# Kernel optimization log

Measured on AMD Instinct MI355X. Metric: run time of the kernel, lower is better.

Reference implementation:

```python
import jax, jax.numpy as jnp
import numpy as np

VOCAB = 50000
D = 300
S = 5
CTX = 10
B = 16384

def setup_inputs() -> dict:
    key = jax.random.key(0)
    k1, k2, k3 = jax.random.split(key, 3)
    x = jax.random.randint(k1, (B, 2 + CTX), 0, VOCAB, dtype=jnp.int32)
    W_g = jax.random.normal(k2, (VOCAB, D), dtype=jnp.float32)
    W_s = jax.random.normal(k3, (VOCAB, S, D), dtype=jnp.float32)
    return {"x": x, "W_g": W_g, "W_s": W_s}

def reference(x, W_g, W_s):
    # sum of context word global vectors: gather (B, CTX, D) -> sum -> (B, D)
    sum_context = jnp.sum(W_g[x[:, 2:]], axis=1)
    # sense vectors of target word: (B, S, D)
    sense_vecs = W_s[x[:, 0]]
    # per-sense dot with context (theano scan over senses): (S, B)
    scores = jnp.einsum('bsd,bd->sb', sense_vecs, sum_context)
    # (right_senses / context_sense_vectors are dead code in the original)
    # literal translation: sigmoid of sum over axis=1 of (S, B) -> (S,)
    return jax.nn.sigmoid(jnp.sum(scores, axis=1))
```

## Files before the change

kernel.cpp:

```cpp
#include <hip/hip_runtime.h>

typedef float v4f __attribute__((ext_vector_type(4)));

#define BATCH 16384
#define NS    5
#define NCTX  10
#define XSTR  (NCTX + 2)
#define D4    75
#define NBLK  4096

__global__ __launch_bounds__(256, 8) void sense_partials(
    const int*   __restrict__ x,
    const float* __restrict__ Wg,
    const float* __restrict__ Ws,
    float*       __restrict__ partial ) {
  const int lane = threadIdx.x & 63;
  const int wid  = threadIdx.x >> 6;
  const int b    = blockIdx.x * 4 + wid;

  const v4f* Wg4 = (const v4f*)Wg;
  const v4f* Ws4 = (const v4f*)Ws;

  int v = (lane < XSTR) ? x[(size_t)b * XSTR + lane] : 0;
  const int w0 = __shfl(v, 0);
  const v4f* wrow = Ws4 + (size_t)w0 * (NS * D4);

  const bool hi = (lane < D4 - 64);

  v4f sc0 = 0.f, sc1 = 0.f;
#pragma unroll
  for (int j = 0; j < NCTX; ++j) {
    const int c = __shfl(v, 2 + j);
    const v4f* r = Wg4 + (size_t)c * D4;
    sc0 += r[lane];
    if (hi) sc1 += r[64 + lane];
  }

  float acc[NS];
#pragma unroll
  for (int s = 0; s < NS; ++s) {
    v4f a0 = __builtin_nontemporal_load(&wrow[s * D4 + lane]);
    v4f p  = a0 * sc0;
    if (hi) {
      v4f a1 = __builtin_nontemporal_load(&wrow[s * D4 + 64 + lane]);
      p += a1 * sc1;
    }
    acc[s] = p.x + p.y + p.z + p.w;
  }

#pragma unroll
  for (int s = 0; s < NS; ++s) {
    float t = acc[s];
#pragma unroll
    for (int off = 32; off; off >>= 1) t += __shfl_down(t, off);
    acc[s] = t;
  }

  __shared__ float red[4][NS];
  if (lane == 0) {
#pragma unroll
    for (int s = 0; s < NS; ++s) red[wid][s] = acc[s];
  }
  __syncthreads();
  if (threadIdx.x < NS) {
    float t = red[0][threadIdx.x] + red[1][threadIdx.x] +
              red[2][threadIdx.x] + red[3][threadIdx.x];
    partial[threadIdx.x * NBLK + blockIdx.x] = t;
  }
}

__global__ __launch_bounds__(320) void sense_reduce(
    const float* __restrict__ partial, float* __restrict__ out) {
  const int lane = threadIdx.x & 63;
  const int s    = threadIdx.x >> 6;
  float sum = 0.f;
  for (int g = lane; g < NBLK; g += 64) sum += partial[s * NBLK + g];
#pragma unroll
  for (int off = 32; off; off >>= 1) sum += __shfl_down(sum, off);
  if (lane == 0) out[s] = 1.0f / (1.0f + __expf(-sum));
}

extern "C" void kernel_launch(void* const* d_in, const int* in_sizes, int n_in,
                              void* d_out, int out_size, void* d_ws, size_t ws_size,
                              hipStream_t stream) {
  const int*   x  = (const int*)d_in[0];
  const float* Wg = (const float*)d_in[1];
  const float* Ws = (const float*)d_in[2];
  float* partial  = (float*)d_ws;
  float* out      = (float*)d_out;

  sense_partials<<<NBLK, 256, 0, stream>>>(x, Wg, Ws, partial);
  sense_reduce<<<1, 320, 0, stream>>>(partial, out);
}
```

Baseline: 412.6 us.

## Process four batch rows per wavefront and pack tail columns across lanes

Each wavefront now handles four batch rows instead of one. The 11 leftover float4 columns of each row, beyond the first 64, are packed into lanes 0-43 so that lane utilization on the tail loads rises from 11/64 to 44/64. This raises memory-level parallelism per wave and cuts the block count to 1024 with lower occupancy bounds. In exchange it uses more registers and leaves fewer waves resident to hide latency.

```diff
diff --git a/kernel.cpp b/kernel.cpp
--- a/kernel.cpp
+++ b/kernel.cpp
@@ -7,44 +7,65 @@
 #define NCTX  10
 #define XSTR  (NCTX + 2)
 #define D4    75
-#define NBLK  4096
+#define HI    11
+#define NBLK  1024
 
-__global__ __launch_bounds__(256, 8) void sense_partials(
+__global__ __launch_bounds__(256, 4) void sense_partials(
     const int*   __restrict__ x,
     const float* __restrict__ Wg,
     const float* __restrict__ Ws,
     float*       __restrict__ partial ) {
   const int lane = threadIdx.x & 63;
   const int wid  = threadIdx.x >> 6;
-  const int b    = blockIdx.x * 4 + wid;
+  const int grp  = blockIdx.x * 4 + wid;
+  const int b0   = grp * 4;
 
   const v4f* Wg4 = (const v4f*)Wg;
   const v4f* Ws4 = (const v4f*)Ws;
 
-  int v = (lane < XSTR) ? x[(size_t)b * XSTR + lane] : 0;
-  const int w0 = __shfl(v, 0);
-  const v4f* wrow = Ws4 + (size_t)w0 * (NS * D4);
+  int v = (lane < 4 * XSTR) ? x[(size_t)b0 * XSTR + lane] : 0;
 
-  const bool hi = (lane < D4 - 64);
+  const int hr = lane / HI;
+  const int hc = lane - hr * HI;
+  const bool hiOn = (lane < 4 * HI);
 
-  v4f sc0 = 0.f, sc1 = 0.f;
+  int w0[4];
+#pragma unroll
+  for (int r = 0; r < 4; ++r) w0[r] = __shfl(v, r * XSTR);
+  const int wH = __shfl(v, hr * XSTR);
+
+  v4f s0[4] = {0.f, 0.f, 0.f, 0.f};
+  v4f sH    = 0.f;
+
 #pragma unroll
   for (int j = 0; j < NCTX; ++j) {
-    const int c = __shfl(v, 2 + j);
-    const v4f* r = Wg4 + (size_t)c * D4;
-    sc0 += r[lane];
-    if (hi) sc1 += r[64 + lane];
+    int c0 = __shfl(v, 0 * XSTR + 2 + j);
+    int c1 = __shfl(v, 1 * XSTR + 2 + j);
+    int c2 = __shfl(v, 2 * XSTR + 2 + j);
+    int c3 = __shfl(v, 3 * XSTR + 2 + j);
+    int cH = __shfl(v, hr * XSTR + 2 + j);
+    s0[0] += Wg4[(size_t)c0 * D4 + lane];
+    s0[1] += Wg4[(size_t)c1 * D4 + lane];
+    s0[2] += Wg4[(size_t)c2 * D4 + lane];
+    s0[3] += Wg4[(size_t)c3 * D4 + lane];
+    if (hiOn) sH += Wg4[(size_t)cH * D4 + 64 + hc];
   }
+
+  const v4f* wb0 = Ws4 + (size_t)w0[0] * (NS * D4);
+  const v4f* wb1 = Ws4 + (size_t)w0[1] * (NS * D4);
+  const v4f* wb2 = Ws4 + (size_t)w0[2] * (NS * D4);
+  const v4f* wb3 = Ws4 + (size_t)w0[3] * (NS * D4);
+  const v4f* wbH = Ws4 + (size_t)wH    * (NS * D4);
 
   float acc[NS];
 #pragma unroll
   for (int s = 0; s < NS; ++s) {
-    v4f a0 = __builtin_nontemporal_load(&wrow[s * D4 + lane]);
-    v4f p  = a0 * sc0;
-    if (hi) {
-      v4f a1 = __builtin_nontemporal_load(&wrow[s * D4 + 64 + lane]);
-      p += a1 * sc1;
-    }
+    v4f p = __builtin_nontemporal_load(&wb0[s * D4 + lane]) * s0[0]
+          + __builtin_nontemporal_load(&wb1[s * D4 + lane]) * s0[1]
+          + __builtin_nontemporal_load(&wb2[s * D4 + lane]) * s0[2]
+          + __builtin_nontemporal_load(&wb3[s * D4 + lane]) * s0[3];
+    if (hiOn)
+      p += __builtin_nontemporal_load(&wbH[s * D4 + 64 + hc]) * sH;
     acc[s] = p.x + p.y + p.z + p.w;
   }
 
```

After: 419.3 us. About the same (+1.6%).
